# Kernel tuning notes

Measured on AMD Instinct MI355X. Metric: run time of the kernel, lower is better.

## Reference

```python
import jax, jax.numpy as jnp
import numpy as np

N_HEAD = 12

def setup_inputs() -> dict:
    key = jax.random.key(0)
    ks = jax.random.split(key, 5)
    B, T, C = 2, 2048, 768
    s = 0.02
    return {
        "x": jax.random.normal(ks[0], (B, T, C), jnp.float32),
        "c_attn_w": jax.random.normal(ks[1], (C, 3 * C), jnp.float32) * s,
        "c_attn_b": jax.random.normal(ks[2], (3 * C,), jnp.float32) * s,
        "c_proj_w": jax.random.normal(ks[3], (C, C), jnp.float32) * s,
        "c_proj_b": jax.random.normal(ks[4], (C,), jnp.float32) * s,
    }

def reference(x, c_attn_w, c_attn_b, c_proj_w, c_proj_b):
    B, T, C = x.shape
    H = N_HEAD
    D = C // H
    qkv = x @ c_attn_w + c_attn_b              # [B,T,3C]
    q, k, v = jnp.split(qkv, 3, axis=-1)
    # [B,T,C] -> [B,H,T,D]
    q = q.reshape(B, T, H, D).transpose(0, 2, 1, 3)
    k = k.reshape(B, T, H, D).transpose(0, 2, 1, 3)
    v = v.reshape(B, T, H, D).transpose(0, 2, 1, 3)
    att = jnp.einsum('bhqd,bhkd->bhqk', q, k) * (1.0 / np.sqrt(D))
    causal = jnp.tril(jnp.ones((T, T), bool))  # [T,T]
    att = jnp.where(causal[None, None], att, jnp.float32(-jnp.inf))
    att = jax.nn.softmax(att, axis=-1)
    y = jnp.einsum('bhqk,bhkd->bhqd', att, v)  # [B,H,T,D]
    y = y.transpose(0, 2, 1, 3).reshape(B, T, C)
    return y @ c_proj_w + c_proj_b
```

## Files before the change

kernel.cpp:

```cpp
#include <hip/hip_runtime.h>
#include <hip/hip_bf16.h>


using half4   = __attribute__((ext_vector_type(4))) _Float16;
using half8   = __attribute__((ext_vector_type(8))) _Float16;
using floatx4 = __attribute__((ext_vector_type(4))) float;

#define T_SEQ 2048
#define NHEAD 12
#define HDIM 64
#define C3 2304
#define CDIM 768
#define BT 4096
#define BH 24

static __device__ inline _Float16 f2h(float f) { return (_Float16)f; }

static __device__ inline void bar_lgkm() {
    __builtin_amdgcn_s_waitcnt(0xc07f);
    __builtin_amdgcn_s_barrier();
}

__global__ __launch_bounds__(256)
void prologue(const float* __restrict__ wa, const float* __restrict__ wp,
              _Float16* __restrict__ wTa, _Float16* __restrict__ wTp) {
    __shared__ float tile[32][33];
    int blk = blockIdx.x, tid = threadIdx.x;
    const float* w; _Float16* wT; int K, N, bx, by;
    if (blk < 1728) { w = wa; wT = wTa; K = CDIM; N = C3; bx = blk % 72; by = blk / 72; }
    else { int b2 = blk - 1728; w = wp; wT = wTp; K = CDIM; N = CDIM; bx = b2 % 24; by = b2 / 24; }
    int tx = tid & 31, ty = tid >> 5;
    #pragma unroll
    for (int j = 0; j < 32; j += 8) {
        int k = by * 32 + ty + j, n = bx * 32 + tx;
        tile[ty + j][tx] = w[(long)k * N + n];
    }
    __syncthreads();
    #pragma unroll
    for (int j = 0; j < 32; j += 8) {
        int nO = bx * 32 + ty + j, kO = by * 32 + tx;
        wT[(long)nO * K + kO] = f2h(tile[tx][ty + j]);
    }
}

__global__ __launch_bounds__(256)
void gemm_qkv(const float* __restrict__ X, const _Float16* __restrict__ Bt,
              const float* __restrict__ bias,
              _Float16* __restrict__ Qb, _Float16* __restrict__ Kb,
              _Float16* __restrict__ Vt) {
    __shared__ __align__(16) _Float16 As[128 * 72];
    __shared__ __align__(16) _Float16 Bs[96 * 72];
    const int K = CDIM;
    int tid = threadIdx.x;
    int m0 = blockIdx.x * 128, n0 = blockIdx.y * 96;
    int w = tid >> 6, l = tid & 63;
    int wm = (w >> 1) * 64, wn = (w & 1) * 48;
    int lr = l & 15, lq = l >> 4;

    int rs = tid >> 3, cs = (tid & 7) * 8;

    floatx4 acc[4][3] = {};

    floatx4 Arf[4][2]; half8 Br[3];
    #pragma unroll
    for (int j = 0; j < 4; ++j) {
        Arf[j][0] = *(const floatx4*)&X[(long)(m0 + j * 32 + rs) * K + cs];
        Arf[j][1] = *(const floatx4*)&X[(long)(m0 + j * 32 + rs) * K + cs + 4];
    }
    #pragma unroll
    for (int j = 0; j < 3; ++j)
        Br[j] = *(const half8*)&Bt[(long)(n0 + j * 32 + rs) * K + cs];

    for (int kb = 0; kb < K; kb += 64) {
        #pragma unroll
        for (int j = 0; j < 4; ++j) {
            half8 h;
            #pragma unroll
            for (int e = 0; e < 4; ++e) { h[e] = f2h(Arf[j][0][e]); h[4 + e] = f2h(Arf[j][1][e]); }
            *(half8*)&As[(j * 32 + rs) * 72 + cs] = h;
        }
        #pragma unroll
        for (int j = 0; j < 3; ++j)
            *(half8*)&Bs[(j * 32 + rs) * 72 + cs] = Br[j];
        bar_lgkm();
        if (kb + 64 < K) {
            #pragma unroll
            for (int j = 0; j < 4; ++j) {
                Arf[j][0] = *(const floatx4*)&X[(long)(m0 + j * 32 + rs) * K + kb + 64 + cs];
                Arf[j][1] = *(const floatx4*)&X[(long)(m0 + j * 32 + rs) * K + kb + 64 + cs + 4];
            }
            #pragma unroll
            for (int j = 0; j < 3; ++j)
                Br[j] = *(const half8*)&Bt[(long)(n0 + j * 32 + rs) * K + kb + 64 + cs];
        }
        #pragma unroll
        for (int kh = 0; kh < 2; ++kh) {
            half8 af[4], bf[3];
            #pragma unroll
            for (int i = 0; i < 4; ++i)
                af[i] = *(const half8*)&As[(wm + i * 16 + lr) * 72 + kh * 32 + lq * 8];
            #pragma unroll
            for (int i = 0; i < 3; ++i)
                bf[i] = *(const half8*)&Bs[(wn + i * 16 + lr) * 72 + kh * 32 + lq * 8];
            #pragma unroll
            for (int mi = 0; mi < 4; ++mi)
                #pragma unroll
                for (int ni = 0; ni < 3; ++ni)
                    acc[mi][ni] = __builtin_amdgcn_mfma_f32_16x16x32_f16(af[mi], bf[ni], acc[mi][ni], 0, 0, 0);
        }
        bar_lgkm();
    }

    int region = n0 / CDIM;
    if (region < 2) {
        _Float16* O = region ? Kb : Qb;
        int nc0 = n0 - region * CDIM + wn;
        #pragma unroll
        for (int mi = 0; mi < 4; ++mi)
            #pragma unroll
            for (int ni = 0; ni < 3; ++ni) {
                int col = nc0 + ni * 16 + lr;
                float bsc = bias[region * CDIM + col];
                #pragma unroll
                for (int r = 0; r < 4; ++r) {
                    int row = m0 + wm + mi * 16 + lq * 4 + r;
                    O[(long)row * CDIM + col] = f2h(acc[mi][ni][r] + bsc);
                }
            }
    } else {
        #pragma unroll
        for (int mi = 0; mi < 4; ++mi)
            #pragma unroll
            for (int ni = 0; ni < 3; ++ni) {
                int cv = n0 - 2 * CDIM + wn + ni * 16 + lr;
                float bsc = bias[2 * CDIM + cv];
                int h = cv >> 6, d = cv & 63;
                int t0 = m0 + wm + mi * 16 + lq * 4;
                int bb = t0 >> 11, t = t0 & 2047;
                half4 hv;
                #pragma unroll
                for (int r = 0; r < 4; ++r) hv[r] = f2h(acc[mi][ni][r] + bsc);
                *(half4*)&Vt[(((long)bb * NHEAD + h) * HDIM + d) * T_SEQ + t] = hv;
            }
    }
}

__global__ __launch_bounds__(256)
void gemm_proj(const _Float16* __restrict__ A, const _Float16* __restrict__ Bt,
               const float* __restrict__ bias, float* __restrict__ Cout) {
    __shared__ __align__(16) _Float16 As[64 * 72];
    __shared__ __align__(16) _Float16 Bs[96 * 72];
    const int K = CDIM, N = CDIM;
    int tid = threadIdx.x;
    int m0 = blockIdx.x * 64, n0 = blockIdx.y * 96;
    int w = tid >> 6, l = tid & 63;
    int wm = (w >> 1) * 32, wn = (w & 1) * 48;
    int lr = l & 15, lq = l >> 4;

    int rs = tid >> 3, cs = (tid & 7) * 8;

    floatx4 acc[2][3] = {};

    half8 Ar[2], Br[3];
    #pragma unroll
    for (int j = 0; j < 2; ++j)
        Ar[j] = *(const half8*)&A[(long)(m0 + j * 32 + rs) * K + cs];
    #pragma unroll
    for (int j = 0; j < 3; ++j)
        Br[j] = *(const half8*)&Bt[(long)(n0 + j * 32 + rs) * K + cs];

    for (int kb = 0; kb < K; kb += 64) {
        #pragma unroll
        for (int j = 0; j < 2; ++j)
            *(half8*)&As[(j * 32 + rs) * 72 + cs] = Ar[j];
        #pragma unroll
        for (int j = 0; j < 3; ++j)
            *(half8*)&Bs[(j * 32 + rs) * 72 + cs] = Br[j];
        bar_lgkm();
        if (kb + 64 < K) {
            #pragma unroll
            for (int j = 0; j < 2; ++j)
                Ar[j] = *(const half8*)&A[(long)(m0 + j * 32 + rs) * K + kb + 64 + cs];
            #pragma unroll
            for (int j = 0; j < 3; ++j)
                Br[j] = *(const half8*)&Bt[(long)(n0 + j * 32 + rs) * K + kb + 64 + cs];
        }
        #pragma unroll
        for (int kh = 0; kh < 2; ++kh) {
            half8 af[2], bf[3];
            #pragma unroll
            for (int i = 0; i < 2; ++i)
                af[i] = *(const half8*)&As[(wm + i * 16 + lr) * 72 + kh * 32 + lq * 8];
            #pragma unroll
            for (int i = 0; i < 3; ++i)
                bf[i] = *(const half8*)&Bs[(wn + i * 16 + lr) * 72 + kh * 32 + lq * 8];
            #pragma unroll
            for (int mi = 0; mi < 2; ++mi)
                #pragma unroll
                for (int ni = 0; ni < 3; ++ni)
                    acc[mi][ni] = __builtin_amdgcn_mfma_f32_16x16x32_f16(af[mi], bf[ni], acc[mi][ni], 0, 0, 0);
        }
        bar_lgkm();
    }
    #pragma unroll
    for (int mi = 0; mi < 2; ++mi)
        #pragma unroll
        for (int ni = 0; ni < 3; ++ni) {
            int col = n0 + wn + ni * 16 + lr;
            float b = bias[col];
            #pragma unroll
            for (int r = 0; r < 4; ++r) {
                int row = m0 + wm + mi * 16 + lq * 4 + r;
                Cout[(long)row * N + col] = acc[mi][ni][r] + b;
            }
        }
}

__global__ __launch_bounds__(256)
void attn_kernel(const _Float16* __restrict__ Qb, const _Float16* __restrict__ Kb,
                 const _Float16* __restrict__ Vt, _Float16* __restrict__ y) {
    __shared__ __align__(16) _Float16 Ks[128 * 72];
    __shared__ __align__(16) _Float16 Vs[64 * 136];
    __shared__ __align__(16) _Float16 Ps[64 * 136];
    int tid = threadIdx.x;
    int w = tid >> 6, l = tid & 63;
    int lr = l & 15, lq = l >> 4;
    int qs = (w & 1) * 32;
    int kh2 = (w >> 1) * 64;
    int i = blockIdx.x;
    int round = i >> 8, c = i & 255;
    int r_ = (round == 0) ? c : (round == 1 ? 767 - c : 256 + c);
    int qb = 31 - r_ / 24;
    int bh = r_ % 24;
    int b = bh / NHEAD, h = bh % NHEAD;

    const _Float16* Qp = Qb + (long)b * T_SEQ * CDIM + h * HDIM;
    const _Float16* Kg = Kb + (long)b * T_SEQ * CDIM + h * HDIM;
    const _Float16* Vg = Vt + (long)bh * HDIM * T_SEQ;

    int kr = tid >> 3, kc = (tid & 7) * 8;
    int vr = tid >> 4, vc = (tid & 15) * 8;

    const float qscale = 0.125f * 1.44269504f;
    half8 aq[2][2];
    #pragma unroll
    for (int st = 0; st < 2; ++st)
        #pragma unroll
        for (int kk = 0; kk < 2; ++kk) {
            aq[st][kk] = *(const half8*)&Qp[(long)(qb * 64 + qs + st * 16 + lr) * CDIM + kk * 32 + lq * 8];
            #pragma unroll
            for (int j = 0; j < 8; ++j) aq[st][kk][j] = f2h((float)aq[st][kk][j] * qscale);
        }

    int nk = (qb + 2) >> 1;

    half8 Kr[4], Vr[4];
    #pragma unroll
    for (int j = 0; j < 4; ++j) {
        Kr[j] = *(const half8*)&Kg[(long)(j * 32 + kr) * CDIM + kc];
        Vr[j] = *(const half8*)&Vg[(long)(j * 16 + vr) * T_SEQ + vc];
    }

    float psum[2] = {0.f, 0.f};
    floatx4 acc[4][2] = {};
    int qrow0 = qb * 64 + qs + lr, qrow1 = qb * 64 + qs + 16 + lr;

    for (int kt = 0; kt < nk; ++kt) {
        int kbase = kt * 128;
        #pragma unroll
        for (int j = 0; j < 4; ++j) {
            *(half8*)&Ks[(j * 32 + kr) * 72 + kc] = Kr[j];
            *(half8*)&Vs[(j * 16 + vr) * 136 + vc] = Vr[j];
        }
        bar_lgkm();
        if (kt + 1 < nk) {
            int nb = kbase + 128;
            #pragma unroll
            for (int j = 0; j < 4; ++j) {
                Kr[j] = *(const half8*)&Kg[(long)(nb + j * 32 + kr) * CDIM + kc];
                Vr[j] = *(const half8*)&Vg[(long)(j * 16 + vr) * T_SEQ + nb + vc];
            }
        }

        floatx4 sacc[4][2];
        #pragma unroll
        for (int s = 0; s < 4; ++s)
            #pragma unroll
            for (int st = 0; st < 2; ++st) sacc[s][st] = floatx4{0.f, 0.f, 0.f, 0.f};
        #pragma unroll
        for (int s = 0; s < 4; ++s) {
            #pragma unroll
            for (int kk = 0; kk < 2; ++kk) {
                half8 bk = *(const half8*)&Ks[(kh2 + s * 16 + lr) * 72 + kk * 32 + lq * 8];
                sacc[s][0] = __builtin_amdgcn_mfma_f32_16x16x32_f16(bk, aq[0][kk], sacc[s][0], 0, 0, 0);
                sacc[s][1] = __builtin_amdgcn_mfma_f32_16x16x32_f16(bk, aq[1][kk], sacc[s][1], 0, 0, 0);
            }
        }

        if (kt == nk - 1) {
            #pragma unroll
            for (int s = 0; s < 4; ++s) {
                half4 hv0, hv1;
                #pragma unroll
                for (int r = 0; r < 4; ++r) {
                    int key = kbase + kh2 + s * 16 + lq * 4 + r;
                    float p0 = (key > qrow0) ? 0.f : __builtin_amdgcn_exp2f(sacc[s][0][r]);
                    float p1 = (key > qrow1) ? 0.f : __builtin_amdgcn_exp2f(sacc[s][1][r]);
                    psum[0] += p0; psum[1] += p1;
                    hv0[r] = f2h(p0); hv1[r] = f2h(p1);
                }
                *(half4*)&Ps[(qs + lr) * 136 + kh2 + s * 16 + lq * 4] = hv0;
                *(half4*)&Ps[(qs + 16 + lr) * 136 + kh2 + s * 16 + lq * 4] = hv1;
            }
        } else {
            #pragma unroll
            for (int s = 0; s < 4; ++s) {
                half4 hv0, hv1;
                #pragma unroll
                for (int r = 0; r < 4; ++r) {
                    float p0 = __builtin_amdgcn_exp2f(sacc[s][0][r]);
                    float p1 = __builtin_amdgcn_exp2f(sacc[s][1][r]);
                    psum[0] += p0; psum[1] += p1;
                    hv0[r] = f2h(p0); hv1[r] = f2h(p1);
                }
                *(half4*)&Ps[(qs + lr) * 136 + kh2 + s * 16 + lq * 4] = hv0;
                *(half4*)&Ps[(qs + 16 + lr) * 136 + kh2 + s * 16 + lq * 4] = hv1;
            }
        }

        half8 ap[2][2];
        #pragma unroll
        for (int st = 0; st < 2; ++st)
            #pragma unroll
            for (int kk = 0; kk < 2; ++kk)
                ap[st][kk] = *(const half8*)&Ps[(qs + st * 16 + lr) * 136 + kh2 + kk * 32 + lq * 8];
        #pragma unroll
        for (int n = 0; n < 4; ++n) {
            #pragma unroll
            for (int kk = 0; kk < 2; ++kk) {
                half8 bv = *(const half8*)&Vs[(n * 16 + lr) * 136 + kh2 + kk * 32 + lq * 8];
                acc[n][0] = __builtin_amdgcn_mfma_f32_16x16x32_f16(ap[0][kk], bv, acc[n][0], 0, 0, 0);
                acc[n][1] = __builtin_amdgcn_mfma_f32_16x16x32_f16(ap[1][kk], bv, acc[n][1], 0, 0, 0);
            }
        }
        bar_lgkm();
    }

    float* red = (float*)Ks;
    int slot = ((w & 1) * 64 + l) * 36;
    if (w >= 2) {
        #pragma unroll
        for (int n = 0; n < 4; ++n)
            #pragma unroll
            for (int st = 0; st < 2; ++st)
                *(floatx4*)&red[slot + (n * 2 + st) * 4] = acc[n][st];
        red[slot + 32] = psum[0];
        red[slot + 33] = psum[1];
    }
    __syncthreads();
    if (w < 2) {
        #pragma unroll
        for (int n = 0; n < 4; ++n)
            #pragma unroll
            for (int st = 0; st < 2; ++st) {
                floatx4 t = *(const floatx4*)&red[slot + (n * 2 + st) * 4];
                acc[n][st][0] += t[0]; acc[n][st][1] += t[1];
                acc[n][st][2] += t[2]; acc[n][st][3] += t[3];
            }
        psum[0] += red[slot + 32];
        psum[1] += red[slot + 33];

        #pragma unroll
        for (int st = 0; st < 2; ++st) {
            float L = psum[st];
            L += __shfl_xor(L, 16, 64);
            L += __shfl_xor(L, 32, 64);
            float Lr[4];
            #pragma unroll
            for (int r = 0; r < 4; ++r) Lr[r] = __shfl(L, lq * 4 + r, 64);
            #pragma unroll
            for (int n = 0; n < 4; ++n)
                #pragma unroll
                for (int r = 0; r < 4; ++r) {
                    int row = qb * 64 + qs + st * 16 + lq * 4 + r;
                    float v = acc[n][st][r] / Lr[r];
                    y[((long)(b * T_SEQ) + row) * CDIM + h * HDIM + n * 16 + lr] = f2h(v);
                }
        }
    }
}

extern "C" void kernel_launch(void* const* d_in, const int* in_sizes, int n_in,
                              void* d_out, int out_size, void* d_ws, size_t ws_size,
                              hipStream_t stream) {
    const float* x      = (const float*)d_in[0];
    const float* w_attn = (const float*)d_in[1];
    const float* b_attn = (const float*)d_in[2];
    const float* w_proj = (const float*)d_in[3];
    const float* b_proj = (const float*)d_in[4];
    float* out = (float*)d_out;

    char* ws = (char*)d_ws;
    _Float16* wTa = (_Float16*)(ws + 6291456);
    _Float16* wTp = (_Float16*)(ws + 9830400);
    _Float16* Qb  = (_Float16*)(ws + 11010048);
    _Float16* Kb  = (_Float16*)(ws + 17301504);
    _Float16* Vt  = (_Float16*)(ws + 23592960);
    _Float16* yb  = (_Float16*)(ws + 29884416);

    prologue<<<2304, 256, 0, stream>>>(w_attn, w_proj, wTa, wTp);

    gemm_qkv<<<dim3(BT / 128, C3 / 96), 256, 0, stream>>>(x, wTa, b_attn, Qb, Kb, Vt);

    attn_kernel<<<BH * (T_SEQ / 64), 256, 0, stream>>>(Qb, Kb, Vt, yb);

    gemm_proj<<<dim3(BT / 64, CDIM / 96), 256, 0, stream>>>(yb, wTp, b_proj, out);
}
```

Measured before the change: 144.4 us.

## Keep softmax probabilities in registers by permuting V layout in LDS

Removes the P shared-memory round trip. The S accumulator fragment is reused directly as the B operand of the PV MFMA, computing O^T = V^T P^T, with the V tile stored in LDS under a permuted column order so the key indices match. The output is now transposed per lane, which allows 4-wide fp16 stores and a single reciprocal instead of per-element shuffles and divides. This cuts LDS traffic and shared memory, at the cost of split half4 V stores and a subtle index-permutation correctness risk.

Result: faster. 139.3 us, median of 2 (-3.6%).

```diff
diff --git a/kernel.cpp b/kernel.cpp
--- a/kernel.cpp
+++ b/kernel.cpp
@@ -221,7 +221,6 @@
                  const _Float16* __restrict__ Vt, _Float16* __restrict__ y) {
     __shared__ __align__(16) _Float16 Ks[128 * 72];
     __shared__ __align__(16) _Float16 Vs[64 * 136];
-    __shared__ __align__(16) _Float16 Ps[64 * 136];
     int tid = threadIdx.x;
     int w = tid >> 6, l = tid & 63;
     int lr = l & 15, lq = l >> 4;
@@ -240,6 +239,7 @@
 
     int kr = tid >> 3, kc = (tid & 7) * 8;
     int vr = tid >> 4, vc = (tid & 15) * 8;
+    int vpc = (vc & ~31) + ((vc >> 3) & 1) * 16 + ((vc >> 4) & 1) * 4;
 
     const float qscale = 0.125f * 1.44269504f;
     half8 aq[2][2];
@@ -270,7 +270,11 @@
         #pragma unroll
         for (int j = 0; j < 4; ++j) {
             *(half8*)&Ks[(j * 32 + kr) * 72 + kc] = Kr[j];
-            *(half8*)&Vs[(j * 16 + vr) * 136 + vc] = Vr[j];
+            half4 lo, hi;
+            #pragma unroll
+            for (int e = 0; e < 4; ++e) { lo[e] = Vr[j][e]; hi[e] = Vr[j][4 + e]; }
+            *(half4*)&Vs[(j * 16 + vr) * 136 + vpc] = lo;
+            *(half4*)&Vs[(j * 16 + vr) * 136 + vpc + 8] = hi;
         }
         bar_lgkm();
         if (kt + 1 < nk) {
@@ -297,50 +301,43 @@
             }
         }
 
+        half4 ph[2][4];
         if (kt == nk - 1) {
             #pragma unroll
-            for (int s = 0; s < 4; ++s) {
-                half4 hv0, hv1;
+            for (int s = 0; s < 4; ++s)
                 #pragma unroll
                 for (int r = 0; r < 4; ++r) {
                     int key = kbase + kh2 + s * 16 + lq * 4 + r;
                     float p0 = (key > qrow0) ? 0.f : __builtin_amdgcn_exp2f(sacc[s][0][r]);
                     float p1 = (key > qrow1) ? 0.f : __builtin_amdgcn_exp2f(sacc[s][1][r]);
                     psum[0] += p0; psum[1] += p1;
-                    hv0[r] = f2h(p0); hv1[r] = f2h(p1);
+                    ph[0][s][r] = f2h(p0); ph[1][s][r] = f2h(p1);
                 }
-                *(half4*)&Ps[(qs + lr) * 136 + kh2 + s * 16 + lq * 4] = hv0;
-                *(half4*)&Ps[(qs + 16 + lr) * 136 + kh2 + s * 16 + lq * 4] = hv1;
-            }
         } else {
             #pragma unroll
-            for (int s = 0; s < 4; ++s) {
-                half4 hv0, hv1;
+            for (int s = 0; s < 4; ++s)
                 #pragma unroll
                 for (int r = 0; r < 4; ++r) {
                     float p0 = __builtin_amdgcn_exp2f(sacc[s][0][r]);
                     float p1 = __builtin_amdgcn_exp2f(sacc[s][1][r]);
                     psum[0] += p0; psum[1] += p1;
-                    hv0[r] = f2h(p0); hv1[r] = f2h(p1);
+                    ph[0][s][r] = f2h(p0); ph[1][s][r] = f2h(p1);
                 }
-                *(half4*)&Ps[(qs + lr) * 136 + kh2 + s * 16 + lq * 4] = hv0;
-                *(half4*)&Ps[(qs + 16 + lr) * 136 + kh2 + s * 16 + lq * 4] = hv1;
-            }
-        }
-
-        half8 ap[2][2];
-        #pragma unroll
-        for (int st = 0; st < 2; ++st)
-            #pragma unroll
-            for (int kk = 0; kk < 2; ++kk)
-                ap[st][kk] = *(const half8*)&Ps[(qs + st * 16 + lr) * 136 + kh2 + kk * 32 + lq * 8];
-        #pragma unroll
-        for (int n = 0; n < 4; ++n) {
-            #pragma unroll
-            for (int kk = 0; kk < 2; ++kk) {
-                half8 bv = *(const half8*)&Vs[(n * 16 + lr) * 136 + kh2 + kk * 32 + lq * 8];
-                acc[n][0] = __builtin_amdgcn_mfma_f32_16x16x32_f16(ap[0][kk], bv, acc[n][0], 0, 0, 0);
-                acc[n][1] = __builtin_amdgcn_mfma_f32_16x16x32_f16(ap[1][kk], bv, acc[n][1], 0, 0, 0);
+        }
+
+        #pragma unroll
+        for (int kk = 0; kk < 2; ++kk) {
+            half8 bp0, bp1;
+            #pragma unroll
+            for (int e = 0; e < 4; ++e) {
+                bp0[e] = ph[0][2 * kk][e];     bp0[4 + e] = ph[0][2 * kk + 1][e];
+                bp1[e] = ph[1][2 * kk][e];     bp1[4 + e] = ph[1][2 * kk + 1][e];
+            }
+            #pragma unroll
+            for (int n = 0; n < 4; ++n) {
+                half8 av = *(const half8*)&Vs[(n * 16 + lr) * 136 + kh2 + kk * 32 + lq * 8];
+                acc[n][0] = __builtin_amdgcn_mfma_f32_16x16x32_f16(av, bp0, acc[n][0], 0, 0, 0);
+                acc[n][1] = __builtin_amdgcn_mfma_f32_16x16x32_f16(av, bp1, acc[n][1], 0, 0, 0);
             }
         }
         bar_lgkm();
@@ -375,17 +372,15 @@
             float L = psum[st];
             L += __shfl_xor(L, 16, 64);
             L += __shfl_xor(L, 32, 64);
-            float Lr[4];
-            #pragma unroll
-            for (int r = 0; r < 4; ++r) Lr[r] = __shfl(L, lq * 4 + r, 64);
-            #pragma unroll
-            for (int n = 0; n < 4; ++n)
-                #pragma unroll
-                for (int r = 0; r < 4; ++r) {
-                    int row = qb * 64 + qs + st * 16 + lq * 4 + r;
-                    float v = acc[n][st][r] / Lr[r];
-                    y[((long)(b * T_SEQ) + row) * CDIM + h * HDIM + n * 16 + lr] = f2h(v);
-                }
+            float inv = 1.f / L;
+            #pragma unroll
+            for (int n = 0; n < 4; ++n) {
+                half4 hv;
+                #pragma unroll
+                for (int r = 0; r < 4; ++r) hv[r] = f2h(acc[n][st][r] * inv);
+                int row = qb * 64 + qs + st * 16 + lr;
+                *(half4*)&y[((long)(b * T_SEQ) + row) * CDIM + h * HDIM + n * 16 + lq * 4] = hv;
+            }
         }
     }
 }
```
